# Kernel optimization log

Measured on AMD Instinct MI355X. Metric: run time of the kernel, lower is better.

The kernel has to match this reference:

```python
import jax, jax.numpy as jnp
import numpy as np

N, M, C = 262144, 1048576, 32768
ORIG, AF, NF, GH, H, NG = 200, 64, 32, 16, 128, 3


def setup_inputs() -> dict:
    key = jax.random.key(0)
    ks = jax.random.split(key, 16)
    w = lambda k, s: (jax.random.normal(k, s) * 0.02).astype(jnp.float32)
    d = {}
    d["atom_weights"] = jax.random.uniform(ks[0], (N, 1), dtype=jnp.float32)
    d["orig_atom_fea"] = jax.random.normal(ks[1], (N, ORIG), dtype=jnp.float32)
    d["nbr_fea"] = jax.random.normal(ks[2], (M, NF), dtype=jnp.float32)
    d["self_fea_idx"] = jax.random.randint(ks[3], (M,), 0, N)
    d["nbr_fea_idx"] = jax.random.randint(ks[4], (M,), 0, N)
    d["crystal_atom_idx"] = jnp.sort(jax.random.randint(ks[5], (N,), 0, C))
    d["emb_W"] = w(ks[6], (ORIG, AF)); d["emb_b"] = jnp.zeros((AF,), jnp.float32)
    d["filt_W"] = w(ks[7], (NG, 2 * AF + NF, AF)); d["filt_b"] = jnp.zeros((NG, AF), jnp.float32)
    d["core_W"] = w(ks[8], (NG, 2 * AF + NF, AF)); d["core_b"] = jnp.zeros((NG, AF), jnp.float32)
    d["bn_f_g"] = jnp.ones((NG, AF), jnp.float32); d["bn_f_b"] = jnp.zeros((NG, AF), jnp.float32)
    d["bn_c_g"] = jnp.ones((NG, AF), jnp.float32); d["bn_c_b"] = jnp.zeros((NG, AF), jnp.float32)
    d["bn_o_g"] = jnp.ones((NG, AF), jnp.float32); d["bn_o_b"] = jnp.zeros((NG, AF), jnp.float32)
    d["gate_W1"] = w(ks[9], (AF, GH)); d["gate_b1"] = jnp.zeros((GH,), jnp.float32)
    d["gate_bn_g"] = jnp.ones((GH,), jnp.float32); d["gate_bn_b"] = jnp.zeros((GH,), jnp.float32)
    d["gate_W2"] = w(ks[10], (GH, 1)); d["gate_b2"] = jnp.zeros((1,), jnp.float32)
    d["fc_W"] = w(ks[11], (AF, H)); d["fc_b"] = jnp.zeros((H,), jnp.float32)
    d["fc_bn_g"] = jnp.ones((H,), jnp.float32); d["fc_bn_b"] = jnp.zeros((H,), jnp.float32)
    d["out_W"] = w(ks[12], (H, 1)); d["out_b"] = jnp.zeros((1,), jnp.float32)
    return d


def _bn(x, g, b, eps=1e-5):
    # training-mode BatchNorm1d: batch stats over dim 0, biased variance
    return (x - x.mean(0)) / jnp.sqrt(x.var(0) + eps) * g + b


def reference(atom_weights, orig_atom_fea, nbr_fea, self_fea_idx, nbr_fea_idx, crystal_atom_idx,
              emb_W, emb_b, filt_W, filt_b, core_W, core_b,
              bn_f_g, bn_f_b, bn_c_g, bn_c_b, bn_o_g, bn_o_b,
              gate_W1, gate_b1, gate_bn_g, gate_bn_b, gate_W2, gate_b2,
              fc_W, fc_b, fc_bn_g, fc_bn_b, out_W, out_b):
    atom = orig_atom_fea @ emb_W + emb_b  # (N, AF)
    cnt = jnp.clip(jax.ops.segment_sum(jnp.ones((M,), atom.dtype), self_fea_idx, N), 1.0)
    for i in range(NG):  # message-passing layers
        total = jnp.concatenate([atom[self_fea_idx], atom[nbr_fea_idx], nbr_fea], axis=1)  # (M, 2AF+NF)
        f = jax.nn.sigmoid(_bn(total @ filt_W[i] + filt_b[i], bn_f_g[i], bn_f_b[i]))
        c = jax.nn.softplus(_bn(total @ core_W[i] + core_b[i], bn_c_g[i], bn_c_b[i]))
        mean = jax.ops.segment_sum(f * c, self_fea_idx, N) / cnt[:, None]  # scatter_mean
        atom = jax.nn.softplus(atom + _bn(mean, bn_o_g[i], bn_o_b[i]))
    # GlobalAttention pooling over crystals
    gate = jax.nn.relu(_bn(atom @ gate_W1 + gate_b1, gate_bn_g, gate_bn_b)) @ gate_W2 + gate_b2  # (N,1)
    gmax = jax.ops.segment_max(gate, crystal_atom_idx, C)
    gate = atom_weights * jnp.exp(gate - gmax[crystal_atom_idx])
    gate = gate / (jax.ops.segment_sum(gate, crystal_atom_idx, C)[crystal_atom_idx] + 1e-13)
    crys = jax.ops.segment_sum(gate * atom, crystal_atom_idx, C)  # (C, AF)
    crys = jax.nn.softplus(_bn(crys @ fc_W + fc_b, fc_bn_g, fc_bn_b))
    return crys @ out_W + out_b  # (C, 1)
```

## Files before the change

### kernel.cpp

```cpp
#include <hip/hip_runtime.h>
#include <hip/hip_fp16.h>
#include <cstdint>
#include <cstddef>

#define NATOM 262144
#define MEDGE 1048576
#define NCRY  32768

typedef __attribute__((ext_vector_type(8))) short short8v;
typedef __attribute__((ext_vector_type(4))) float f32x4;

__device__ __forceinline__ float4 ld4(const float* p){ return *reinterpret_cast<const float4*>(p); }

__device__ __forceinline__ float softplusf_(float x){
  return fmaxf(x, 0.0f) + log1pf(expf(-fabsf(x)));
}
__device__ __forceinline__ float softplus_fast(float x){
  return fmaxf(x, 0.0f) + __logf(1.0f + __expf(-fabsf(x)));
}
__device__ __forceinline__ float sigmoid_fast(float y){
  return __builtin_amdgcn_rcpf(1.0f + __expf(-y));
}

__device__ __forceinline__ unsigned short rne_bf16(float f){
  unsigned u = __float_as_uint(f);
  unsigned r = u + 0x7FFFu + ((u >> 16) & 1u);
  return (unsigned short)(r >> 16);
}
__device__ __forceinline__ float bfu(short s){
  return __uint_as_float(((unsigned)(unsigned short)s) << 16);
}

__device__ __forceinline__ unsigned fkey(float x){
  unsigned b = __float_as_uint(x);
  return (b & 0x80000000u) ? ~b : (b | 0x80000000u);
}
__device__ __forceinline__ float fkeyinv(unsigned k){
  unsigned b = (k & 0x80000000u) ? (k & 0x7fffffffu) : ~k;
  return __uint_as_float(b);
}

__device__ __forceinline__ void gll16(const void* g, void* l){
  __builtin_amdgcn_global_load_lds((const __attribute__((address_space(1))) unsigned*)g,
                                   (__attribute__((address_space(3))) unsigned*)l, 16, 0, 0);
}

#define CSB 32
__global__ __launch_bounds__(256) void colstage(const float* __restrict__ part,
                                                float* __restrict__ part2, int nb){
  int t = threadIdx.x;
  int rpb = nb / CSB;
  const float* p = part + (size_t)blockIdx.x*rpb*256 + t;
  float s = 0.f;
  #pragma unroll 4
  for (int r = 0; r < rpb; ++r) s += p[(size_t)r*256];
  part2[blockIdx.x*256 + t] = s;
}

__global__ __launch_bounds__(256) void hist_kernel(const int* __restrict__ sidx, int* __restrict__ cnti){
  for (int m = blockIdx.x*256 + threadIdx.x; m < MEDGE; m += gridDim.x*256)
    atomicAdd(&cnti[sidx[m]], 1);
}

__global__ __launch_bounds__(256) void scan1(const int* __restrict__ cnti,
                                             int* __restrict__ loc, int* __restrict__ bsum){
  __shared__ int sm[256];
  int t = threadIdx.x;
  int v = cnti[blockIdx.x*256 + t];
  sm[t] = v;
  __syncthreads();
  for (int off = 1; off < 256; off <<= 1){
    int x = (t >= off) ? sm[t-off] : 0;
    __syncthreads();
    sm[t] += x;
    __syncthreads();
  }
  loc[blockIdx.x*256 + t] = sm[t] - v;
  if (t == 255) bsum[blockIdx.x] = sm[255];
}

__global__ __launch_bounds__(256) void scan2(int* __restrict__ bsum){
  __shared__ int sm[256];
  int t = threadIdx.x;
  int v0 = bsum[t*4+0], v1 = bsum[t*4+1], v2 = bsum[t*4+2], v3 = bsum[t*4+3];
  int tot = v0+v1+v2+v3;
  sm[t] = tot;
  __syncthreads();
  for (int off = 1; off < 256; off <<= 1){
    int x = (t >= off) ? sm[t-off] : 0;
    __syncthreads();
    sm[t] += x;
    __syncthreads();
  }
  int te = sm[t] - tot;
  bsum[t*4+0] = te;
  bsum[t*4+1] = te + v0;
  bsum[t*4+2] = te + v0 + v1;
  bsum[t*4+3] = te + v0 + v1 + v2;
}

__global__ __launch_bounds__(256) void scan3(const int* __restrict__ loc, const int* __restrict__ bsum,
                                             int* __restrict__ base){
  int i = blockIdx.x*256 + threadIdx.x;
  base[i] = loc[i] + bsum[i >> 8];
}

__global__ __launch_bounds__(256) void recip_int(const int* __restrict__ cnti, float* __restrict__ recip){
  int n = blockIdx.x*256 + threadIdx.x;
  if (n < NATOM) recip[n] = 1.0f / fmaxf((float)cnti[n], 1.0f);
}

__global__ __launch_bounds__(256) void rank_kernel(const int* __restrict__ sidx, const int* __restrict__ nidx,
                                                   const int* __restrict__ base, int* __restrict__ ctr,
                                                   const float* __restrict__ nbr,
                                                   int* __restrict__ sidx_s, int* __restrict__ nidx_s,
                                                   short* __restrict__ feap){
  for (int m = blockIdx.x*256 + threadIdx.x; m < MEDGE; m += gridDim.x*256){
    int s = sidx[m];
    int p = base[s] + atomicAdd(&ctr[s], 1);
    sidx_s[p] = s;
    nidx_s[p] = nidx[m];
    const float* src = nbr + (size_t)m*32;
    uint4* dst = (uint4*)(feap + (size_t)p*32);
    #pragma unroll
    for (int c = 0; c < 4; ++c){
      float4 a = ld4(src + c*8), b = ld4(src + c*8 + 4);
      float fv[8] = {a.x,a.y,a.z,a.w,b.x,b.y,b.z,b.w};
      unsigned w[4];
      #pragma unroll
      for (int i=0;i<4;i++)
        w[i] = (unsigned)rne_bf16(fv[2*i]) | ((unsigned)rne_bf16(fv[2*i+1]) << 16);
      dst[c] = make_uint4(w[0],w[1],w[2],w[3]);
    }
  }
}

__global__ __launch_bounds__(256) void wprep_embed(const float* __restrict__ embW,
                                                   short* __restrict__ Weh, short* __restrict__ Wel){
  int idx = blockIdx.x*256 + threadIdx.x;
  if (idx >= 64*224) return;
  int k = idx % 224, c = idx / 224;
  float w = (k < 200) ? embW[(size_t)k*64 + c] : 0.0f;
  unsigned u = __float_as_uint(w);
  unsigned h = u & 0xFFFF0000u;
  Weh[idx] = (short)(h >> 16);
  Wel[idx] = (short)rne_bf16(w - __uint_as_float(h));
}

__global__ __launch_bounds__(256) void embed_mfma(const float* __restrict__ orig,
                                                  const short* __restrict__ Weh,
                                                  const short* __restrict__ Wel,
                                                  const float* __restrict__ bias,
                                                  short* __restrict__ atom_h,
                                                  short* __restrict__ atom_l){
  __shared__ uint4 ab4[3208];
  char* ab = (char*)ab4;
  int t = threadIdx.x, lane = t & 63, wid = t >> 6;
  int r16 = lane & 15, g = lane >> 4;
  int col = wid*16 + r16;

  short8v Bh[7], Bl[7];
  #pragma unroll
  for (int ks = 0; ks < 7; ks++){
    int o = col*224 + ks*32 + g*8;
    Bh[ks] = *(const short8v*)(Weh + o);
    Bl[ks] = *(const short8v*)(Wel + o);
  }
  float bv = bias[col];
  int n0 = blockIdx.x * 64;
  const char* src = (const char*)orig + (size_t)n0*800;
  #pragma unroll
  for (int i = 0; i < 13; i++){
    int j = wid + i*4;
    if (j < 50) gll16(src + j*1024 + lane*16, ab + j*1024);
  }
  __syncthreads();

  #pragma unroll
  for (int grp = 0; grp < 4; grp++){
    f32x4 acc = {bv, bv, bv, bv};
    const char* arow = ab + (grp*16 + r16)*800;
    #pragma unroll
    for (int ks = 0; ks < 7; ks++){
      short8v ah, al;
      if (ks < 6 || g == 0){
        const float* f = (const float*)(arow + ks*128 + g*32);
        float4 f0 = *(const float4*)f, f1 = *(const float4*)(f+4);
        float fv[8] = {f0.x,f0.y,f0.z,f0.w,f1.x,f1.y,f1.z,f1.w};
        unsigned hw[4], lw[4];
        #pragma unroll
        for (int p = 0; p < 4; p++){
          unsigned ua = __float_as_uint(fv[2*p]), ub = __float_as_uint(fv[2*p+1]);
          unsigned ha = ua & 0xFFFF0000u, hb = ub & 0xFFFF0000u;
          hw[p] = (ha >> 16) | hb;
          lw[p] = (unsigned)rne_bf16(fv[2*p]   - __uint_as_float(ha))
                | ((unsigned)rne_bf16(fv[2*p+1] - __uint_as_float(hb)) << 16);
        }
        ah = __builtin_bit_cast(short8v, make_uint4(hw[0],hw[1],hw[2],hw[3]));
        al = __builtin_bit_cast(short8v, make_uint4(lw[0],lw[1],lw[2],lw[3]));
      } else {
        ah = (short8v)0; al = (short8v)0;
      }
      acc = __builtin_amdgcn_mfma_f32_16x16x32_bf16(ah, Bh[ks], acc, 0, 0, 0);
      acc = __builtin_amdgcn_mfma_f32_16x16x32_bf16(al, Bh[ks], acc, 0, 0, 0);
      acc = __builtin_amdgcn_mfma_f32_16x16x32_bf16(ah, Bl[ks], acc, 0, 0, 0);
    }
    int rowb = n0 + grp*16 + g*4;
    #pragma unroll
    for (int r = 0; r < 4; r++){
      float a = acc[r];
      unsigned u = __float_as_uint(a), h = u & 0xFFFF0000u;
      size_t off = (size_t)(rowb + r)*64 + col;
      atom_h[off] = (short)(h >> 16);
      atom_l[off] = (short)rne_bf16(a - __uint_as_float(h));
    }
  }
}

__global__ __launch_bounds__(256) void wprep(const float* __restrict__ filtW, const float* __restrict__ coreW,
                                             short* __restrict__ Wth, short* __restrict__ Wtl){
  int idx = blockIdx.x*256 + threadIdx.x;
  if (idx >= 3*128*160) return;
  int k = idx % 160; int rest = idx / 160; int c = rest & 127; int layer = rest >> 7;
  float w = (c < 64) ? filtW[((size_t)layer*160 + k)*64 + c] : coreW[((size_t)layer*160 + k)*64 + (c-64)];
  unsigned u = __float_as_uint(w);
  unsigned h = u & 0xFFFF0000u;
  Wth[idx] = (short)(h >> 16);
  Wtl[idx] = (short)rne_bf16(w - __uint_as_float(h));
}

#define NT_PER_BLK 8

#define MFMA_B(A,B,ACC) ACC = __builtin_amdgcn_mfma_f32_16x16x32_bf16(A, B, ACC, 0, 0, 0)

template<int PASS>
__global__ __launch_bounds__(256) void edge_mfma(
    const short* __restrict__ atom_h, const short* __restrict__ atom_l,
    const short* __restrict__ nbr_h,
    const int* __restrict__ sidx, const int* __restrict__ nidx,
    const short* __restrict__ Wth, const short* __restrict__ Wtl,
    const float* __restrict__ bfp, const float* __restrict__ bcp,
    const float* __restrict__ scale, const float* __restrict__ shift,
    float* __restrict__ partial,
    float* __restrict__ meanacc,
    unsigned short* __restrict__ ycache)
{
  __shared__ uint4 xb[2][36*32];
  int t = threadIdx.x, lane = t & 63, wid = t >> 6;
  int r16 = lane & 15, g = lane >> 4;
  int colf = wid*16 + r16, colc = colf + 64;
  int el = lane & 31;

  short8v Bhf[5], Blf[5], Bhc[5], Blc[5];
  {
    const short* wfh = Wth + colf*160;
    const short* wch = Wth + colc*160;
    const short* wfl = Wtl + colf*160;
    const short* wcl = Wtl + colc*160;
    #pragma unroll
    for (int ks = 0; ks < 5; ks++){
      int o = ks*32 + g*8;
      Bhf[ks] = *(const short8v*)(wfh + o);
      Bhc[ks] = *(const short8v*)(wch + o);
      Blf[ks] = *(const short8v*)(wfl + o);
      Blc[ks] = *(const short8v*)(wcl + o);
    }
  }
  float bfv = bfp[colf], bcv = bcp[colf];
  float sf = 0.f, hf = 0.f, sc = 0.f, hc = 0.f;
  if (PASS == 1){ sf = scale[colf]; hf = shift[colf]; sc = scale[colc]; hc = shift[colc]; }
  float s0 = 0.f, q0 = 0.f, s1 = 0.f, q1 = 0.f;

  int tile0 = blockIdx.x * NT_PER_BLK;

  #define STAGE(BUF, TILE, SE, NE)                                              \
  {                                                                             \
    uint4* dst = (uint4*)(BUF);                                                 \
    int e0s_ = (TILE)*32;                                                       \
    _Pragma("unroll")                                                           \
    for (int j = wid; j < 18; j += 4){                                          \
      int c = 2*j + (lane >> 5);                                                \
      const short* src;                                                         \
      if      (c < 8)  src = atom_h + (size_t)(SE)*64 + c*8;                    \
      else if (c < 16) src = atom_h + (size_t)(NE)*64 + (c-8)*8;                \
      else if (c < 20) src = nbr_h + (size_t)(e0s_+el)*32 + (c-16)*8;           \
      else if (c < 28) src = atom_l + (size_t)(SE)*64 + (c-20)*8;               \
      else             src = atom_l + (size_t)(NE)*64 + (c-28)*8;               \
      gll16(src, dst + j*64);                                                   \
    }                                                                           \
  }

  int se, ne;
  { int e = tile0*32 + el; se = sidx[e]; ne = nidx[e]; }
  STAGE(xb[0], tile0, se, ne);
  { int e = (tile0+1)*32 + el; se = sidx[e]; ne = nidx[e]; }

  for (int tt = 0; tt < NT_PER_BLK; ++tt){
    asm volatile("s_waitcnt vmcnt(0)" ::: "memory");
    __builtin_amdgcn_s_barrier();
    if (tt+1 < NT_PER_BLK){
      STAGE(xb[(tt+1)&1], tile0+tt+1, se, ne);
      if (tt+2 < NT_PER_BLK){ int e = (tile0+tt+2)*32 + el; se = sidx[e]; ne = nidx[e]; }
    }
    int e0 = (tile0+tt)*32;
    const char* buf = (const char*)xb[tt & 1];
    #pragma unroll
    for (int grp = 0; grp < 2; ++grp){
      f32x4 accf = {bfv,bfv,bfv,bfv}, accc = {bcv,bcv,bcv,bcv};
      const char* base = buf + (grp*16 + r16)*16;
      #pragma unroll
      for (int ks = 0; ks < 5; ++ks){
        short8v ah = *(const short8v*)(base + (ks*4+g)*512);
        MFMA_B(ah, Bhf[ks], accf); MFMA_B(ah, Bhc[ks], accc);
        MFMA_B(ah, Blf[ks], accf); MFMA_B(ah, Blc[ks], accc);
        if (ks < 4){
          short8v al = *(const short8v*)(base + (20+ks*4+g)*512);
          MFMA_B(al, Bhf[ks], accf); MFMA_B(al, Bhc[ks], accc);
        }
      }
      if (PASS == 0){
        #pragma unroll
        for (int r = 0; r < 4; r++){
          float yf = accf[r], yc = accc[r];
          s0 += yf; q0 += yf*yf; s1 += yc; q1 += yc*yc;
        }
        if (ycache){
          int ebase = e0 + grp*16 + g*4;
          uint2 pf, pc;
          #pragma unroll
          for (int r = 0; r < 4; r++){
            ((__half*)&pf)[r] = __float2half_rn(accf[r]);
            ((__half*)&pc)[r] = __float2half_rn(accc[r]);
          }
          uint2* yrow = (uint2*)ycache + (size_t)(ebase >> 2)*128;
          yrow[colf]      = pf;
          yrow[64 + colf] = pc;
        }
      } else {
        int ebase = e0 + grp*16 + g*4;
        int a_prev = sidx[ebase];
        float accum = 0.f;
        #pragma unroll
        for (int r = 0; r < 4; r++){
          float f  = sigmoid_fast(accf[r]*sf + hf);
          float c2 = softplus_fast(accc[r]*sc + hc);
          int a = sidx[ebase + r];
          if (a != a_prev){
            atomicAdd(&meanacc[(size_t)a_prev*64 + colf], accum);
            accum = 0.f;
            a_prev = a;
          }
          accum += f*c2;
        }
        atomicAdd(&meanacc[(size_t)a_prev*64 + colf], accum);
      }
    }
  }
  #undef STAGE

  if (PASS == 0){
    s0 += __shfl_xor(s0,16); s0 += __shfl_xor(s0,32);
    q0 += __shfl_xor(q0,16); q0 += __shfl_xor(q0,32);
    s1 += __shfl_xor(s1,16); s1 += __shfl_xor(s1,32);
    q1 += __shfl_xor(q1,16); q1 += __shfl_xor(q1,32);
    __syncthreads();
    float* scm = (float*)&xb[0][0];
    if (g == 0)
      *(float4*)&scm[(wid*16 + r16)*4] = make_float4(s0, q0, s1, q1);
    __syncthreads();
    {
      int stat = t >> 7, colx = t & 127;
      int isc = (colx >= 64) ? 1 : 0;
      int cc = colx & 63;
      int v = isc*2 + stat;
      partial[(size_t)blockIdx.x*256 + stat*128 + colx] = scm[((cc>>4)*16 + (cc&15))*4 + v];
    }
  }
}

__global__ __launch_bounds__(256) void edge_actv(const unsigned short* __restrict__ ycache,
                                                 const int* __restrict__ sidx_s,
                                                 const float* __restrict__ scale,
                                                 const float* __restrict__ shift,
                                                 float* __restrict__ meanacc){
  int j = threadIdx.x & 63;
  int q = threadIdx.x >> 6;
  float sf = scale[j], hf = shift[j];
  float sc = scale[j+64], hc = shift[j+64];
  for (int eq = blockIdx.x*4 + q; eq < MEDGE/4; eq += gridDim.x*4){
    const uint2* yrow = (const uint2*)ycache + (size_t)eq*128;
    uint2 f4 = yrow[j];
    uint2 c4 = yrow[64 + j];
    const int* sp = sidx_s + eq*4;
    int a_prev = sp[0];
    float accum = 0.f;
    #pragma unroll
    for (int r = 0; r < 4; ++r){
      float yf = __half2float(((const __half*)&f4)[r]);
      float yc = __half2float(((const __half*)&c4)[r]);
      float f  = sigmoid_fast(yf*sf + hf);
      float c2 = softplus_fast(yc*sc + hc);
      int a = sp[r];
      if (a != a_prev){
        atomicAdd(&meanacc[(size_t)a_prev*64 + j], accum);
        accum = 0.f;
        a_prev = a;
      }
      accum += f*c2;
    }
    atomicAdd(&meanacc[(size_t)a_prev*64 + j], accum);
  }
}

__global__ void bnfin_kernel(int nf, float invcnt, const float* __restrict__ p2,
                             const float* __restrict__ g, const float* __restrict__ b,
                             float* __restrict__ scale, float* __restrict__ shift){
  int j = threadIdx.x;
  if (j >= nf) return;
  float s = 0.f, q = 0.f;
  #pragma unroll 4
  for (int r = 0; r < CSB; ++r){
    s += p2[r*256 + j];
    q += p2[r*256 + 128 + j];
  }
  float m = s*invcnt;
  float v = fmaxf(q*invcnt - m*m, 0.0f);
  float is = rsqrtf(v + 1e-5f);
  float sc = g[j]*is;
  scale[j] = sc;
  shift[j] = b[j] - m*sc;
}

__global__ void bnfin2_kernel(float invcnt, const float* __restrict__ p2,
                              const float* __restrict__ g0, const float* __restrict__ b0,
                              const float* __restrict__ g1, const float* __restrict__ b1,
                              float* __restrict__ scale, float* __restrict__ shift){
  int j = threadIdx.x;
  float s = 0.f, q = 0.f;
  #pragma unroll 4
  for (int r = 0; r < CSB; ++r){
    s += p2[r*256 + j];
    q += p2[r*256 + 128 + j];
  }
  float m = s*invcnt;
  float v = fmaxf(q*invcnt - m*m, 0.0f);
  float is = rsqrtf(v + 1e-5f);
  float gg = (j < 64) ? g0[j] : g1[j-64];
  float bb = (j < 64) ? b0[j] : b1[j-64];
  float sc = gg*is;
  scale[j] = sc;
  shift[j] = bb - m*sc;
}

__global__ __launch_bounds__(256) void meanbn_stats(const float* __restrict__ recip,
                                                    const float* __restrict__ meanacc,
                                                    float* __restrict__ partial){
  int t = threadIdx.x;
  float s = 0.f, q = 0.f;
  for (size_t idx = (size_t)blockIdx.x*256 + t; idx < (size_t)NATOM*64; idx += (size_t)gridDim.x*256){
    int n = (int)(idx >> 6);
    float v = meanacc[idx]*recip[n];
    s += v; q += v*v;
  }
  __shared__ float red[256][2];
  red[t][0]=s; red[t][1]=q;
  __syncthreads();
  if (t < 64){
    for (int i=1;i<4;i++){ s += red[t+64*i][0]; q += red[t+64*i][1]; }
    partial[(size_t)blockIdx.x*256 + t]       = s;
    partial[(size_t)blockIdx.x*256 + 128 + t] = q;
  }
}

__global__ __launch_bounds__(256) void atom_update(short* __restrict__ atom_h,
                                                   short* __restrict__ atom_l,
                                                   float* __restrict__ meanacc,
                                                   const float* __restrict__ recip,
                                                   const float* __restrict__ scale,
                                                   const float* __restrict__ shift){
  for (size_t idx = (size_t)blockIdx.x*256 + threadIdx.x; idx < (size_t)NATOM*64; idx += (size_t)gridDim.x*256){
    int n = (int)(idx >> 6), j = (int)(idx & 63);
    float prev = bfu(atom_h[idx]) + bfu(atom_l[idx]);
    float a = softplus_fast(prev + meanacc[idx]*recip[n]*scale[j] + shift[j]);
    meanacc[idx] = 0.0f;
    unsigned u = __float_as_uint(a), h = u & 0xFFFF0000u;
    atom_h[idx] = (short)(h >> 16);
    atom_l[idx] = (short)rne_bf16(a - __uint_as_float(h));
  }
}

__global__ __launch_bounds__(256, 2) void gate_pass1(const short* __restrict__ atom_h,
                                                     const short* __restrict__ atom_l,
                                                     const float* __restrict__ W1, const float* __restrict__ b1,
                                                     float* __restrict__ hbuf,
                                                     float* __restrict__ partial){
  __shared__ float As[256*65];
  __shared__ float Wl[64*16];
  int t = threadIdx.x;
  *(float4*)&Wl[t*4] = ld4(W1 + t*4);
  const short* hsrc = atom_h + (size_t)blockIdx.x*256*64;
  const short* lsrc = atom_l + (size_t)blockIdx.x*256*64;
  #pragma unroll
  for (int j = 0; j < 8; j++){
    int idx = j*256 + t;
    uint4 hv = *(const uint4*)(hsrc + idx*8);
    uint4 lv = *(const uint4*)(lsrc + idx*8);
    int r = idx >> 3, c = (idx & 7)*8;
    float* d = &As[r*65 + c];
    unsigned hw[4] = {hv.x,hv.y,hv.z,hv.w}, lw[4] = {lv.x,lv.y,lv.z,lv.w};
    #pragma unroll
    for (int i = 0; i < 4; i++){
      d[2*i]   = __uint_as_float(hw[i] << 16)          + __uint_as_float(lw[i] << 16);
      d[2*i+1] = __uint_as_float(hw[i] & 0xFFFF0000u)  + __uint_as_float(lw[i] & 0xFFFF0000u);
    }
  }
  __syncthreads();
  float h[16];
  #pragma unroll
  for (int c=0;c<16;c++) h[c] = b1[c];
  const float* ar = &As[t*65];
  #pragma unroll 8
  for (int k=0;k<64;k++){
    float a = ar[k];
    #pragma unroll
    for (int c=0;c<16;c++) h[c] += a*Wl[k*16+c];
  }
  size_t n = (size_t)blockIdx.x*256 + t;
  #pragma unroll
  for (int c=0;c<16;c+=4)
    *(float4*)&hbuf[n*16+c] = make_float4(h[c],h[c+1],h[c+2],h[c+3]);
  __syncthreads();
  #pragma unroll
  for (int c=0;c<16;c++){
    float v = h[c], v2 = h[c]*h[c];
    for (int off=32; off; off>>=1){ v += __shfl_down(v,off); v2 += __shfl_down(v2,off); }
    if ((t&63)==0){ As[(t>>6)*32 + c] = v; As[(t>>6)*32 + 16 + c] = v2; }
  }
  __syncthreads();
  if (t < 32){
    float v = As[t] + As[32+t] + As[64+t] + As[96+t];
    int col = (t < 16) ? t : (128 + t - 16);
    partial[(size_t)blockIdx.x*256 + col] = v;
  }
}

__global__ __launch_bounds__(256) void gate_pass2(const float* __restrict__ hbuf,
                                                  const float* __restrict__ scale, const float* __restrict__ shift,
                                                  const float* __restrict__ W2, const float* __restrict__ b2,
                                                  const int* __restrict__ cry,
                                                  float* __restrict__ gate, unsigned* __restrict__ gmaxk){
  int n = blockIdx.x*256 + threadIdx.x;
  float g = b2[0];
  #pragma unroll
  for (int c=0;c<16;c+=4){
    float4 hv = ld4(hbuf + (size_t)n*16 + c);
    float4 sc = ld4(scale + c), sh = ld4(shift + c), w = ld4(W2 + c);
    g += fmaxf(hv.x*sc.x+sh.x,0.f)*w.x + fmaxf(hv.y*sc.y+sh.y,0.f)*w.y
       + fmaxf(hv.z*sc.z+sh.z,0.f)*w.z + fmaxf(hv.w*sc.w+sh.w,0.f)*w.w;
  }
  gate[n] = g;
  atomicMax(&gmaxk[cry[n]], fkey(g));
}

__global__ __launch_bounds__(256) void gate_exp(float* __restrict__ gate,
                                                const float* __restrict__ aw,
                                                const int* __restrict__ cry,
                                                const unsigned* __restrict__ gmaxk,
                                                float* __restrict__ gsum){
  int n = blockIdx.x*256 + threadIdx.x;
  if (n < NATOM){
    int c = cry[n];
    float w = aw[n]*expf(gate[n] - fkeyinv(gmaxk[c]));
    gate[n] = w;
    atomicAdd(&gsum[c], w);
  }
}

__global__ __launch_bounds__(256) void crys_acc(const float* __restrict__ gate,
                                                const float* __restrict__ gsum,
                                                const int* __restrict__ cry,
                                                const short* __restrict__ atom_h,
                                                const short* __restrict__ atom_l,
                                                float* __restrict__ crys){
  for (size_t idx = (size_t)blockIdx.x*256 + threadIdx.x; idx < (size_t)NATOM*64; idx += (size_t)gridDim.x*256){
    int n = (int)(idx >> 6), j = (int)(idx & 63);
    int c = cry[n];
    float wn = gate[n] / (gsum[c] + 1e-13f);
    float a = bfu(atom_h[idx]) + bfu(atom_l[idx]);
    atomicAdd(&crys[(size_t)c*64 + j], wn*a);
  }
}

__global__ __launch_bounds__(512) void fc_stats(const float* __restrict__ crys,
                                                const float* __restrict__ fcW, const float* __restrict__ fcb,
                                                float* __restrict__ hid,
                                                float* __restrict__ partial){
  __shared__ float Wl[64*128];
  __shared__ float cb[64][16];
  int t = threadIdx.x;
  for (int j = t; j < 64*32; j += 512)
    *(float4*)&Wl[j*4] = ld4(fcW + j*4);
  int cg = t & 31, cr = t >> 5;
  float4 bias = ld4(fcb + cg*4);
  float ssum[4] = {0,0,0,0}, ssq[4] = {0,0,0,0};
  for (int chunk = blockIdx.x; chunk < NCRY/16; chunk += gridDim.x){
    int c0 = chunk*16;
    __syncthreads();
    for (int j = t; j < 256; j += 512){
      int rr = j & 15, c = j >> 4;
      float4 v = ld4(crys + (size_t)(c0+rr)*64 + c*4);
      int k = c*4;
      cb[k][rr]=v.x; cb[k+1][rr]=v.y; cb[k+2][rr]=v.z; cb[k+3][rr]=v.w;
    }
    __syncthreads();
    float4 acc = bias;
    #pragma unroll 4
    for (int k=0;k<64;k++){
      float a = cb[k][cr];
      float4 w = *(float4*)&Wl[k*128 + cg*4];
      acc.x += a*w.x; acc.y += a*w.y; acc.z += a*w.z; acc.w += a*w.w;
    }
    *(float4*)&hid[(size_t)(c0+cr)*128 + cg*4] = acc;
    ssum[0]+=acc.x; ssum[1]+=acc.y; ssum[2]+=acc.z; ssum[3]+=acc.w;
    ssq[0]+=acc.x*acc.x; ssq[1]+=acc.y*acc.y; ssq[2]+=acc.z*acc.z; ssq[3]+=acc.w*acc.w;
  }
  __syncthreads();
  float* red = Wl;
  #pragma unroll
  for (int q=0;q<4;q++){ red[t*8+q] = ssum[q]; red[t*8+4+q] = ssq[q]; }
  __syncthreads();
  if (t < 128){
    int cgj = t >> 2, q = t & 3;
    float s = 0.f, sq = 0.f;
    for (int cri=0; cri<16; cri++){
      int tt = cri*32 + cgj;
      s  += red[tt*8+q];
      sq += red[tt*8+4+q];
    }
    partial[(size_t)blockIdx.x*256 + t]       = s;
    partial[(size_t)blockIdx.x*256 + 128 + t] = sq;
  }
}

__global__ __launch_bounds__(256) void out_kernel(const float* __restrict__ hid,
                                                  const float* __restrict__ scale, const float* __restrict__ shift,
                                                  const float* __restrict__ outW, const float* __restrict__ outb,
                                                  float* __restrict__ out){
  int c = blockIdx.x*4 + (threadIdx.x >> 6);
  int l = threadIdx.x & 63;
  float v = softplusf_(hid[(size_t)c*128 + l]*scale[l] + shift[l])*outW[l]
          + softplusf_(hid[(size_t)c*128 + 64 + l]*scale[64+l] + shift[64+l])*outW[64+l];
  for (int off=32; off; off >>= 1) v += __shfl_down(v, off);
  if (l == 0) out[c] = v + outb[0];
}

extern "C" void kernel_launch(void* const* d_in, const int* in_sizes, int n_in,
                              void* d_out, int out_size, void* d_ws, size_t ws_size,
                              hipStream_t stream){
  const float* aw    = (const float*)d_in[0];
  const float* orig  = (const float*)d_in[1];
  const float* nbr   = (const float*)d_in[2];
  const int*   sidx  = (const int*)d_in[3];
  const int*   nidx  = (const int*)d_in[4];
  const int*   cry   = (const int*)d_in[5];
  const float* embW  = (const float*)d_in[6];
  const float* embB  = (const float*)d_in[7];
  const float* filtW = (const float*)d_in[8];
  const float* filtB = (const float*)d_in[9];
  const float* coreW = (const float*)d_in[10];
  const float* coreB = (const float*)d_in[11];
  const float* bnfg  = (const float*)d_in[12];
  const float* bnfb  = (const float*)d_in[13];
  const float* bncg  = (const float*)d_in[14];
  const float* bncb  = (const float*)d_in[15];
  const float* bnog  = (const float*)d_in[16];
  const float* bnob  = (const float*)d_in[17];
  const float* gW1   = (const float*)d_in[18];
  const float* gb1   = (const float*)d_in[19];
  const float* gbng  = (const float*)d_in[20];
  const float* gbnb  = (const float*)d_in[21];
  const float* gW2   = (const float*)d_in[22];
  const float* gb2   = (const float*)d_in[23];
  const float* fcW   = (const float*)d_in[24];
  const float* fcb   = (const float*)d_in[25];
  const float* fcbng = (const float*)d_in[26];
  const float* fcbnb = (const float*)d_in[27];
  const float* outW  = (const float*)d_in[28];
  const float* outb  = (const float*)d_in[29];
  float* out = (float*)d_out;

  float* ws      = (float*)d_ws;
  float* meanacc = ws;
  float* cnt     = meanacc + (size_t)NATOM*64;
  float* gate    = cnt     + NATOM;
  float* gmaxk   = gate    + NATOM;
  float* gsum    = gmaxk   + NCRY;
  float* crys    = gsum    + NCRY;
  float* hid     = crys    + (size_t)NCRY*64;
  float* part2   = hid     + (size_t)NCRY*128;
  float* scale   = part2   + 32*256;
  float* shift   = scale   + 128;
  short* wth     = (short*)(shift + 128);
  short* wtl     = wth + 3*128*160;
  float* partial = (float*)(wtl + 3*128*160);
  short* atom_h  = (short*)(partial + 4096*256);
  short* atom_l  = atom_h + (size_t)NATOM*64;
  short* weh     = atom_l + (size_t)NATOM*64;
  short* wel     = weh + 64*224;
  short* feap    = wel + 64*224;
  int*   cnti    = (int*)(feap + (size_t)MEDGE*32);
  int*   loc     = cnti + NATOM;
  int*   base    = loc + NATOM;
  int*   ctr     = base + NATOM;
  int*   bsum    = ctr + NATOM;
  int*   sidx_s  = bsum + 1024;
  int*   nidx_s  = sidx_s + MEDGE;
  unsigned short* ycache = (unsigned short*)(nidx_s + MEDGE);
  size_t need = (size_t)((char*)(ycache + (size_t)MEDGE*128) - (char*)d_ws);
  bool use_yc = (ws_size >= need);
  unsigned short* yc = use_yc ? ycache : nullptr;
  (void)in_sizes; (void)n_in; (void)out_size;

  hipMemsetAsync(cnti, 0, NATOM*sizeof(int), stream);
  hipMemsetAsync(ctr, 0, NATOM*sizeof(int), stream);
  hipMemsetAsync(meanacc, 0, (size_t)NATOM*64*sizeof(float), stream);
  hist_kernel<<<2048, 256, 0, stream>>>(sidx, cnti);
  scan1<<<NATOM/256, 256, 0, stream>>>(cnti, loc, bsum);
  scan2<<<1, 256, 0, stream>>>(bsum);
  scan3<<<NATOM/256, 256, 0, stream>>>(loc, bsum, base);
  recip_int<<<NATOM/256, 256, 0, stream>>>(cnti, cnt);
  wprep<<<240, 256, 0, stream>>>(filtW, coreW, wth, wtl);
  wprep_embed<<<56, 256, 0, stream>>>(embW, weh, wel);
  rank_kernel<<<2048, 256, 0, stream>>>(sidx, nidx, base, ctr, nbr, sidx_s, nidx_s, feap);
  embed_mfma<<<NATOM/64, 256, 0, stream>>>(orig, weh, wel, embB, atom_h, atom_l);

  for (int i = 0; i < 3; ++i){
    const short* wthL = wth + (size_t)i*128*160;
    const short* wtlL = wtl + (size_t)i*128*160;
    const float* bf = filtB + i*64;
    const float* bc = coreB + i*64;
    edge_mfma<0><<<4096, 256, 0, stream>>>(atom_h, atom_l, feap, sidx_s, nidx_s, wthL, wtlL, bf, bc,
                                           nullptr, nullptr, partial, nullptr, yc);
    colstage<<<CSB, 256, 0, stream>>>(partial, part2, 4096);
    bnfin2_kernel<<<1, 128, 0, stream>>>(1.0f/MEDGE, part2,
                                         bnfg+i*64, bnfb+i*64, bncg+i*64, bncb+i*64, scale, shift);
    if (use_yc){
      edge_actv<<<2048, 256, 0, stream>>>(ycache, sidx_s, scale, shift, meanacc);
    } else {
      edge_mfma<1><<<4096, 256, 0, stream>>>(atom_h, atom_l, feap, sidx_s, nidx_s, wthL, wtlL, bf, bc,
                                             scale, shift, nullptr, meanacc, nullptr);
    }
    meanbn_stats<<<2048, 256, 0, stream>>>(cnt, meanacc, partial);
    colstage<<<CSB, 256, 0, stream>>>(partial, part2, 2048);
    bnfin_kernel<<<1, 64, 0, stream>>>(64, 1.0f/NATOM, part2, bnog+i*64, bnob+i*64, scale, shift);
    atom_update<<<2048, 256, 0, stream>>>(atom_h, atom_l, meanacc, cnt, scale, shift);
  }

  float* hbuf = meanacc;
  gate_pass1<<<NATOM/256, 256, 0, stream>>>(atom_h, atom_l, gW1, gb1, hbuf, partial);
  colstage<<<CSB, 256, 0, stream>>>(partial, part2, NATOM/256);
  bnfin_kernel<<<1, 16, 0, stream>>>(16, 1.0f/NATOM, part2, gbng, gbnb, scale, shift);
  hipMemsetAsync(gmaxk, 0, NCRY*sizeof(unsigned), stream);
  gate_pass2<<<NATOM/256, 256, 0, stream>>>(hbuf, scale, shift, gW2, gb2, cry, gate, (unsigned*)gmaxk);
  hipMemsetAsync(gsum, 0, NCRY*sizeof(float), stream);
  gate_exp<<<NATOM/256, 256, 0, stream>>>(gate, aw, cry, (const unsigned*)gmaxk, gsum);
  hipMemsetAsync(crys, 0, (size_t)NCRY*64*sizeof(float), stream);
  crys_acc<<<4096, 256, 0, stream>>>(gate, gsum, cry, atom_h, atom_l, crys);

  fc_stats<<<1024, 512, 0, stream>>>(crys, fcW, fcb, hid, partial);
  colstage<<<CSB, 256, 0, stream>>>(partial, part2, 1024);
  bnfin_kernel<<<1, 128, 0, stream>>>(128, 1.0f/NCRY, part2, fcbng, fcbnb, scale, shift);
  out_kernel<<<NCRY/4, 256, 0, stream>>>(hid, scale, shift, outW, outb, out);
}
```

Before: 1.434 ms.

## Replace atomic edge scatter with per-atom CSR gather fused with mean BN stats

Swaps the atomic scatter-add over sorted edges for a gather: each wavefront walks its atoms' contiguous edge ranges in the sorted cache using base/count offsets. It writes the mean directly and computes the output-BN partial sums in the same pass. This drops the atomics, the memset of the accumulator, the separate stats kernel and the re-zeroing in atom_update. The cost is load imbalance from variable atom degree and partial reads of 4-edge groups that straddle atom boundaries.

After: 1.432 ms. Within noise of the previous version (-0.1%).

```diff
diff --git a/kernel.cpp b/kernel.cpp
--- a/kernel.cpp
+++ b/kernel.cpp
@@ -378,37 +378,49 @@
   }
 }
 
-__global__ __launch_bounds__(256) void edge_actv(const unsigned short* __restrict__ ycache,
-                                                 const int* __restrict__ sidx_s,
+__global__ __launch_bounds__(256) void aggregate(const unsigned short* __restrict__ ycache,
+                                                 const int* __restrict__ base,
+                                                 const int* __restrict__ cnti,
                                                  const float* __restrict__ scale,
                                                  const float* __restrict__ shift,
-                                                 float* __restrict__ meanacc){
-  int j = threadIdx.x & 63;
-  int q = threadIdx.x >> 6;
+                                                 float* __restrict__ meanacc,
+                                                 float* __restrict__ partial){
+  int t = threadIdx.x, j = t & 63, w = t >> 6;
   float sf = scale[j], hf = shift[j];
   float sc = scale[j+64], hc = shift[j+64];
-  for (int eq = blockIdx.x*4 + q; eq < MEDGE/4; eq += gridDim.x*4){
-    const uint2* yrow = (const uint2*)ycache + (size_t)eq*128;
-    uint2 f4 = yrow[j];
-    uint2 c4 = yrow[64 + j];
-    const int* sp = sidx_s + eq*4;
-    int a_prev = sp[0];
-    float accum = 0.f;
-    #pragma unroll
-    for (int r = 0; r < 4; ++r){
-      float yf = __half2float(((const __half*)&f4)[r]);
-      float yc = __half2float(((const __half*)&c4)[r]);
-      float f  = sigmoid_fast(yf*sf + hf);
-      float c2 = softplus_fast(yc*sc + hc);
-      int a = sp[r];
-      if (a != a_prev){
-        atomicAdd(&meanacc[(size_t)a_prev*64 + j], accum);
-        accum = 0.f;
-        a_prev = a;
+  float s = 0.f, q = 0.f;
+  int n0 = blockIdx.x*128 + w*32;
+  for (int i = 0; i < 32; ++i){
+    int n = n0 + i;
+    int b0 = base[n], deg = cnti[n];
+    float acc = 0.f;
+    if (deg > 0){
+      int q0 = b0 >> 2, q1 = (b0 + deg + 3) >> 2;
+      for (int qq = q0; qq < q1; ++qq){
+        const uint2* yrow = (const uint2*)ycache + (size_t)qq*128;
+        uint2 f4 = yrow[j], c4 = yrow[64 + j];
+        int e0 = qq*4;
+        #pragma unroll
+        for (int r = 0; r < 4; ++r){
+          int e = e0 + r;
+          if (e >= b0 && e < b0 + deg){
+            float yf = __half2float(((const __half*)&f4)[r]);
+            float yc = __half2float(((const __half*)&c4)[r]);
+            acc += sigmoid_fast(yf*sf + hf) * softplus_fast(yc*sc + hc);
+          }
+        }
       }
-      accum += f*c2;
-    }
-    atomicAdd(&meanacc[(size_t)a_prev*64 + j], accum);
+    }
+    float mean = acc / fmaxf((float)deg, 1.0f);
+    meanacc[(size_t)n*64 + j] = mean;
+    s += mean; q += mean*mean;
+  }
+  __shared__ float red[4][128];
+  red[w][j] = s; red[w][64+j] = q;
+  __syncthreads();
+  if (t < 64){
+    partial[(size_t)blockIdx.x*256 + t]       = red[0][t]+red[1][t]+red[2][t]+red[3][t];
+    partial[(size_t)blockIdx.x*256 + 128 + t] = red[0][64+t]+red[1][64+t]+red[2][64+t]+red[3][64+t];
   }
 }
 
@@ -472,17 +484,19 @@
   }
 }
 
+template<int PREMUL>
 __global__ __launch_bounds__(256) void atom_update(short* __restrict__ atom_h,
                                                    short* __restrict__ atom_l,
-                                                   float* __restrict__ meanacc,
+                                                   const float* __restrict__ meanacc,
                                                    const float* __restrict__ recip,
                                                    const float* __restrict__ scale,
                                                    const float* __restrict__ shift){
   for (size_t idx = (size_t)blockIdx.x*256 + threadIdx.x; idx < (size_t)NATOM*64; idx += (size_t)gridDim.x*256){
     int n = (int)(idx >> 6), j = (int)(idx & 63);
+    float mv = meanacc[idx];
+    if (PREMUL) mv *= recip[n];
     float prev = bfu(atom_h[idx]) + bfu(atom_l[idx]);
-    float a = softplus_fast(prev + meanacc[idx]*recip[n]*scale[j] + shift[j]);
-    meanacc[idx] = 0.0f;
+    float a = softplus_fast(prev + mv*scale[j] + shift[j]);
     unsigned u = __float_as_uint(a), h = u & 0xFFFF0000u;
     atom_h[idx] = (short)(h >> 16);
     atom_l[idx] = (short)rne_bf16(a - __uint_as_float(h));
@@ -723,7 +737,6 @@
 
   hipMemsetAsync(cnti, 0, NATOM*sizeof(int), stream);
   hipMemsetAsync(ctr, 0, NATOM*sizeof(int), stream);
-  hipMemsetAsync(meanacc, 0, (size_t)NATOM*64*sizeof(float), stream);
   hist_kernel<<<2048, 256, 0, stream>>>(sidx, cnti);
   scan1<<<NATOM/256, 256, 0, stream>>>(cnti, loc, bsum);
   scan2<<<1, 256, 0, stream>>>(bsum);
@@ -745,15 +758,19 @@
     bnfin2_kernel<<<1, 128, 0, stream>>>(1.0f/MEDGE, part2,
                                          bnfg+i*64, bnfb+i*64, bncg+i*64, bncb+i*64, scale, shift);
     if (use_yc){
-      edge_actv<<<2048, 256, 0, stream>>>(ycache, sidx_s, scale, shift, meanacc);
+      aggregate<<<NATOM/128, 256, 0, stream>>>(ycache, base, cnti, scale, shift, meanacc, partial);
+      colstage<<<CSB, 256, 0, stream>>>(partial, part2, NATOM/128);
+      bnfin_kernel<<<1, 64, 0, stream>>>(64, 1.0f/NATOM, part2, bnog+i*64, bnob+i*64, scale, shift);
+      atom_update<0><<<2048, 256, 0, stream>>>(atom_h, atom_l, meanacc, cnt, scale, shift);
     } else {
+      hipMemsetAsync(meanacc, 0, (size_t)NATOM*64*sizeof(float), stream);
       edge_mfma<1><<<4096, 256, 0, stream>>>(atom_h, atom_l, feap, sidx_s, nidx_s, wthL, wtlL, bf, bc,
                                              scale, shift, nullptr, meanacc, nullptr);
-    }
-    meanbn_stats<<<2048, 256, 0, stream>>>(cnt, meanacc, partial);
-    colstage<<<CSB, 256, 0, stream>>>(partial, part2, 2048);
-    bnfin_kernel<<<1, 64, 0, stream>>>(64, 1.0f/NATOM, part2, bnog+i*64, bnob+i*64, scale, shift);
-    atom_update<<<2048, 256, 0, stream>>>(atom_h, atom_l, meanacc, cnt, scale, shift);
+      meanbn_stats<<<2048, 256, 0, stream>>>(cnt, meanacc, partial);
+      colstage<<<CSB, 256, 0, stream>>>(partial, part2, 2048);
+      bnfin_kernel<<<1, 64, 0, stream>>>(64, 1.0f/NATOM, part2, bnog+i*64, bnob+i*64, scale, shift);
+      atom_update<1><<<2048, 256, 0, stream>>>(atom_h, atom_l, meanacc, cnt, scale, shift);
+    }
   }
 
   float* hbuf = meanacc;
```
